# Kernel optimization log

Measured on AMD Instinct MI355X. Metric: run time of the kernel, lower is better.

The kernel has to match this reference:

```python
import jax, jax.numpy as jnp
import numpy as np

N_NODES = 100000
N_EDGES = 1600000
FEAT = 64
HID = 64
N_LAYERS = 3
N_GRAPHS = 500


def setup_inputs() -> dict:
    key = jax.random.key(0)
    ks = jax.random.split(key, 8)
    x = jax.random.normal(ks[0], (N_NODES, FEAT), dtype=jnp.float32)
    edge_index = jax.random.randint(ks[1], (2, N_EDGES), 0, N_NODES, dtype=jnp.int64)
    mask = jax.random.randint(ks[2], (N_NODES,), 0, 2).astype(bool)
    batch = jnp.sort(jax.random.randint(ks[3], (N_NODES,), 0, N_GRAPHS, dtype=jnp.int64))
    Ws = jax.random.normal(ks[4], (N_LAYERS, HID, HID), dtype=jnp.float32) * 0.1
    bs = jnp.zeros((N_LAYERS, HID), dtype=jnp.float32)
    lt1_w = jax.random.normal(ks[5], (HID, 1), dtype=jnp.float32) * 0.1
    lt1_b = jnp.zeros((1,), dtype=jnp.float32)
    return {"x": x, "edge_index": edge_index, "mask": mask, "batch": batch,
            "Ws": Ws, "bs": bs, "lt1_w": lt1_w, "lt1_b": lt1_b}


def reference(x, edge_index, mask, batch, Ws, bs, lt1_w, lt1_b):
    n = x.shape[0]
    self_loop = jnp.arange(n, dtype=edge_index.dtype)
    src = jnp.concatenate([edge_index[0], self_loop])  # [E+N]
    dst = jnp.concatenate([edge_index[1], self_loop])
    # GCN symmetric normalization with self loops
    deg = jax.ops.segment_sum(jnp.ones_like(dst, dtype=x.dtype), dst, num_segments=n)
    dis = jax.lax.rsqrt(deg)  # deg >= 1 thanks to self loops
    norm = (dis[src] * dis[dst])[:, None]  # [E+N, 1]

    h = x
    for i in range(N_LAYERS):
        h = h @ Ws[i]                                   # [N, H] linear (no bias)
        msg = h[src] * norm                              # gather + scale
        h = jax.ops.segment_sum(msg, dst, num_segments=n) + bs[i]  # scatter-add + bias
        h = jax.nn.elu(h)
        # F.dropout with training=False is identity (eval mode)

    # global_mean_pool over masked nodes per graph
    m = mask.astype(h.dtype)
    num = jax.ops.segment_sum(h * m[:, None], batch, num_segments=N_GRAPHS)
    den = jax.ops.segment_sum(m, batch, num_segments=N_GRAPHS)
    pooled = num / jnp.maximum(den, 1.0)[:, None]        # [G, H]
    return pooled @ lt1_w + lt1_b                        # [G, 1]
```

## Files before the change

kernel.cpp:

```cpp
#include <hip/hip_runtime.h>
#include <math.h>

#define N_NODES 100000
#define N_EDGES 1600000
#define HID 64
#define N_LAYERS 3
#define N_GRAPHS 500

#define BUK_SHIFT 9
#define BUK_NODES 512
#define NBUK ((N_NODES + BUK_NODES - 1) / BUK_NODES)
#define BIN_BLOCKS 256
#define CHUNK ((N_EDGES + BIN_BLOCKS - 1) / BIN_BLOCKS)
#define BCAP 16384
#define PCAP 20480

#define TM 64
#define LDX 68

typedef _Float16 half_t;
union H4 { ushort4 u; half_t h[4]; };

__device__ __forceinline__ float elu_f(float x) { return x > 0.f ? x : expm1f(x); }
__device__ __forceinline__ int pad8(int c) { return (c + 7) & ~7; }


__global__ void kA_bin(const int* __restrict__ ei, int* __restrict__ bcur,
                       unsigned int* __restrict__ bin) {
    __shared__ int h[NBUK];
    __shared__ int rsv[NBUK];
    for (int i = threadIdx.x; i < NBUK; i += 256) h[i] = 0;
    __syncthreads();
    int lo = blockIdx.x * CHUNK;
    int hi = min(lo + CHUNK, N_EDGES);
    for (int e = lo + (int)threadIdx.x; e < hi; e += 256)
        atomicAdd(&h[ei[N_EDGES + e] >> BUK_SHIFT], 1);
    __syncthreads();
    for (int i = threadIdx.x; i < NBUK; i += 256) {
        int c = h[i];
        rsv[i] = c ? atomicAdd(&bcur[i], c) : 0;
        h[i] = 0;
    }
    __syncthreads();
    for (int e = lo + (int)threadIdx.x; e < hi; e += 256) {
        int d = ei[N_EDGES + e];
        int s = ei[e];
        int b = d >> BUK_SHIFT;
        int pos = rsv[b] + atomicAdd(&h[b], 1);
        if (pos < BCAP)
            bin[(size_t)b * BCAP + pos] = (unsigned)s | ((unsigned)(d & (BUK_NODES - 1)) << 17);
    }
}

__global__ void kB_build(const unsigned int* __restrict__ bin,
                         const int* __restrict__ bcur,
                         int* __restrict__ poff, int* __restrict__ plen,
                         float* __restrict__ dis, int* __restrict__ psrc,
                         half_t* __restrict__ B16) {
    __shared__ int cnt[BUK_NODES];
    __shared__ int excl[BUK_NODES];
    __shared__ int ps[256];
    int b = blockIdx.x;
    int t = threadIdx.x;
    int ecnt = min(bcur[b], BCAP);
    size_t e0 = (size_t)b * BCAP;
    size_t p0 = (size_t)b * PCAP;
    int n0 = b << BUK_SHIFT;

    if (b == 0 && t < HID) B16[(size_t)N_NODES * HID + t] = (half_t)0.f;

    cnt[t] = 0; cnt[t + 256] = 0;
    __syncthreads();
    for (int e = t; e < ecnt; e += 256)
        atomicAdd(&cnt[bin[e0 + e] >> 17], 1);
    __syncthreads();
    int pc0 = pad8(cnt[2 * t]), pc1 = pad8(cnt[2 * t + 1]);
    int psum = pc0 + pc1;
    ps[t] = psum;
    __syncthreads();
    for (int o = 1; o < 256; o <<= 1) {
        int u = (t >= o) ? ps[t - o] : 0;
        __syncthreads();
        ps[t] += u;
        __syncthreads();
    }
    int pexcl = ps[t] - psum;
    excl[2 * t] = pexcl;
    excl[2 * t + 1] = pexcl + pc0;
    int ptot = ps[255];
    __syncthreads();
    for (int i = t; i < BUK_NODES; i += 256) {
        int n = n0 + i;
        if (n < N_NODES) {
            poff[n] = (int)p0 + excl[i];
            plen[n] = pad8(cnt[i]);
            dis[n] = rsqrtf((float)cnt[i] + 1.0f);
        }
    }
    for (int j = t; j < ptot; j += 256) psrc[p0 + j] = N_NODES;
    __syncthreads();
    cnt[t] = excl[t]; cnt[t + 256] = excl[t + 256];
    __syncthreads();
    for (int e = t; e < ecnt; e += 256) {
        unsigned v = bin[e0 + e];
        int dloc = v >> 17;
        int pos = atomicAdd(&cnt[dloc], 1);
        if (pos < PCAP) psrc[p0 + pos] = (int)(v & 0x1FFFFu);
    }
}


#define FMA4(acc, xs_, wv_) \
    acc.x = fmaf(xs_, wv_.x, acc.x); acc.y = fmaf(xs_, wv_.y, acc.y); \
    acc.z = fmaf(xs_, wv_.z, acc.z); acc.w = fmaf(xs_, wv_.w, acc.w);

__global__ void __launch_bounds__(256, 4)
k_gemm(const float* __restrict__ Xf, const half_t* __restrict__ Xh,
       const float* __restrict__ W, const float* __restrict__ bias, int act,
       const float* __restrict__ dis, half_t* __restrict__ B16, int n) {
    __shared__ float  wsh[HID * LDX];
    __shared__ half_t xs[TM * LDX];
    int t = threadIdx.x;
    int row0 = blockIdx.x * TM;

#pragma unroll
    for (int q = 0; q < 4; q++) {
        int f = q * 1024 + t * 4;
        int r = f >> 6, c = f & 63;
        *(float4*)&wsh[r * LDX + c] = *(const float4*)&W[f];
    }
#pragma unroll
    for (int q = 0; q < 4; q++) {
        int f = q * 1024 + t * 4;
        int r = f >> 6, c = f & 63;
        int gr = row0 + r;
        float4 v = make_float4(0.f, 0.f, 0.f, 0.f);
        if (gr < n) {
            if (act) {
                H4 xu; xu.u = *(const ushort4*)&Xh[(size_t)gr * HID + c];
                float4 bb = *(const float4*)&bias[c];
                v.x = elu_f((float)xu.h[0] + bb.x);
                v.y = elu_f((float)xu.h[1] + bb.y);
                v.z = elu_f((float)xu.h[2] + bb.z);
                v.w = elu_f((float)xu.h[3] + bb.w);
            } else {
                v = *(const float4*)&Xf[(size_t)gr * HID + c];
            }
        }
        H4 pk;
        pk.h[0] = (half_t)v.x; pk.h[1] = (half_t)v.y;
        pk.h[2] = (half_t)v.z; pk.h[3] = (half_t)v.w;
        *(ushort4*)&xs[r * LDX + c] = pk.u;
    }
    __syncthreads();

    int tx = t & 15, ty = t >> 4;
    float4 acc0 = make_float4(0.f, 0.f, 0.f, 0.f);
    float4 acc1 = acc0, acc2 = acc0, acc3 = acc0;

#pragma unroll 1
    for (int k = 0; k < HID; k += 4) {
        float4 w0 = *(const float4*)&wsh[(k + 0) * LDX + 4 * tx];
        float4 w1 = *(const float4*)&wsh[(k + 1) * LDX + 4 * tx];
        float4 w2 = *(const float4*)&wsh[(k + 2) * LDX + 4 * tx];
        float4 w3 = *(const float4*)&wsh[(k + 3) * LDX + 4 * tx];
        {
            H4 xu; xu.u = *(const ushort4*)&xs[(4 * ty + 0) * LDX + k];
            FMA4(acc0, (float)xu.h[0], w0) FMA4(acc0, (float)xu.h[1], w1)
            FMA4(acc0, (float)xu.h[2], w2) FMA4(acc0, (float)xu.h[3], w3)
        }
        {
            H4 xu; xu.u = *(const ushort4*)&xs[(4 * ty + 1) * LDX + k];
            FMA4(acc1, (float)xu.h[0], w0) FMA4(acc1, (float)xu.h[1], w1)
            FMA4(acc1, (float)xu.h[2], w2) FMA4(acc1, (float)xu.h[3], w3)
        }
        {
            H4 xu; xu.u = *(const ushort4*)&xs[(4 * ty + 2) * LDX + k];
            FMA4(acc2, (float)xu.h[0], w0) FMA4(acc2, (float)xu.h[1], w1)
            FMA4(acc2, (float)xu.h[2], w2) FMA4(acc2, (float)xu.h[3], w3)
        }
        {
            H4 xu; xu.u = *(const ushort4*)&xs[(4 * ty + 3) * LDX + k];
            FMA4(acc3, (float)xu.h[0], w0) FMA4(acc3, (float)xu.h[1], w1)
            FMA4(acc3, (float)xu.h[2], w2) FMA4(acc3, (float)xu.h[3], w3)
        }
    }

#pragma unroll
    for (int i = 0; i < 4; i++) {
        float4 a = (i == 0) ? acc0 : (i == 1) ? acc1 : (i == 2) ? acc2 : acc3;
        int gr = row0 + 4 * ty + i;
        if (gr < n) {
            float d = dis[gr];
            H4 pk;
            pk.h[0] = (half_t)(a.x * d); pk.h[1] = (half_t)(a.y * d);
            pk.h[2] = (half_t)(a.z * d); pk.h[3] = (half_t)(a.w * d);
            *(ushort4*)&B16[(size_t)gr * HID + 4 * tx] = pk.u;
        }
    }
}

__global__ void k_agg(const int* __restrict__ poff, const int* __restrict__ plen,
                      const int* __restrict__ psrc,
                      const float* __restrict__ dis, const half_t* __restrict__ B16,
                      half_t* __restrict__ A16, int n) {
    int lane = threadIdx.x & 63;
    int node = __builtin_amdgcn_readfirstlane((blockIdx.x * blockDim.x + threadIdx.x) >> 6);
    if (node >= n) return;
    float acc = (float)B16[(size_t)node * HID + lane];
    int p = poff[node];
    int p1 = p + plen[node];
    for (; p + 16 <= p1; p += 16) {
        int s[16];
#pragma unroll
        for (int i = 0; i < 16; i++) s[i] = psrc[p + i];
        float v[16];
#pragma unroll
        for (int i = 0; i < 16; i++) v[i] = (float)B16[(size_t)s[i] * HID + lane];
        acc += (((v[0] + v[1]) + (v[2] + v[3])) + ((v[4] + v[5]) + (v[6] + v[7])))
             + (((v[8] + v[9]) + (v[10] + v[11])) + ((v[12] + v[13]) + (v[14] + v[15])));
    }
    if (p < p1) {
        int s[8];
#pragma unroll
        for (int i = 0; i < 8; i++) s[i] = psrc[p + i];
        float v[8];
#pragma unroll
        for (int i = 0; i < 8; i++) v[i] = (float)B16[(size_t)s[i] * HID + lane];
        acc += ((v[0] + v[1]) + (v[2] + v[3])) + ((v[4] + v[5]) + (v[6] + v[7]));
    }
    A16[(size_t)node * HID + lane] = (half_t)(acc * dis[node]);
}

__global__ void k_pool_final(const half_t* __restrict__ A16, const float* __restrict__ bias,
                             const int* __restrict__ mask, const int* __restrict__ batch,
                             const float* __restrict__ w, const float* __restrict__ b,
                             float* __restrict__ out) {
    __shared__ float sacc[4][HID];
    __shared__ float scnt[4];
    int g = blockIdx.x;
    int t = threadIdx.x;
    int lane = t & 63;
    int wv = t >> 6;

    int lo = 0, hi = N_NODES;
    while (lo < hi) { int mid = (lo + hi) >> 1; if (batch[mid] < g) lo = mid + 1; else hi = mid; }
    int n0 = lo;
    hi = N_NODES;
    while (lo < hi) { int mid = (lo + hi) >> 1; if (batch[mid] < g + 1) lo = mid + 1; else hi = mid; }
    int n1 = lo;

    float bl = bias[lane];
    float acc0 = 0.f, acc1 = 0.f;
    float cnt0 = 0.f, cnt1 = 0.f;
    int n = n0 + wv;
    for (; n + 4 < n1; n += 8) {
        int m0 = mask[n], m1 = mask[n + 4];
        float v0 = (float)A16[(size_t)n * HID + lane];
        float v1 = (float)A16[(size_t)(n + 4) * HID + lane];
        if (m0) { acc0 += elu_f(v0 + bl); cnt0 += 1.f; }
        if (m1) { acc1 += elu_f(v1 + bl); cnt1 += 1.f; }
    }
    if (n < n1 && mask[n]) { acc0 += elu_f((float)A16[(size_t)n * HID + lane] + bl); cnt0 += 1.f; }
    acc0 += acc1; cnt0 += cnt1;

    sacc[wv][lane] = acc0;
    if (lane == 0) scnt[wv] = cnt0;
    __syncthreads();
    if (wv == 0) {
        float v = sacc[0][lane] + sacc[1][lane] + sacc[2][lane] + sacc[3][lane];
        float c = scnt[0] + scnt[1] + scnt[2] + scnt[3];
        v = v / fmaxf(c, 1.0f) * w[lane];
#pragma unroll
        for (int o = 32; o > 0; o >>= 1) v += __shfl_down(v, o);
        if (lane == 0) out[g] = v + b[0];
    }
}

extern "C" void kernel_launch(void* const* d_in, const int* in_sizes, int n_in,
                              void* d_out, int out_size, void* d_ws, size_t ws_size,
                              hipStream_t stream) {
    const float* x     = (const float*)d_in[0];
    const int*   ei    = (const int*)d_in[1];
    const int*   mask  = (const int*)d_in[2];
    const int*   batch = (const int*)d_in[3];
    const float* Ws    = (const float*)d_in[4];
    const float* bs    = (const float*)d_in[5];
    const float* lw    = (const float*)d_in[6];
    const float* lb    = (const float*)d_in[7];
    float* out = (float*)d_out;

    half_t* A16  = (half_t*)d_ws;
    half_t* B16  = A16 + (size_t)N_NODES * HID;
    float*  dis  = (float*)(B16 + (size_t)(N_NODES + 1) * HID);
    int*    poff = (int*)(dis + N_NODES);
    int*    plen = poff + N_NODES;
    int*    bcur = plen + N_NODES;
    int*    psrc = bcur + NBUK;
    unsigned int* bin = (unsigned int*)(psrc + (size_t)NBUK * PCAP);

    hipMemsetAsync(bcur, 0, NBUK * sizeof(int), stream);

    kA_bin<<<BIN_BLOCKS, 256, 0, stream>>>(ei, bcur, bin);
    kB_build<<<NBUK, 256, 0, stream>>>(bin, bcur, poff, plen, dis, psrc, B16);

    const int gemm_blocks = (N_NODES + TM - 1) / TM;
    const int row_blocks  = (N_NODES + 3) / 4;
    for (int l = 0; l < N_LAYERS; l++) {
        const float* bias_in = (l == 0) ? bs : bs + (l - 1) * HID;
        k_gemm<<<gemm_blocks, 256, 0, stream>>>((l == 0) ? x : nullptr,
                                                (l == 0) ? nullptr : A16,
                                                Ws + (size_t)l * HID * HID,
                                                bias_in, (l == 0) ? 0 : 1,
                                                dis, B16, N_NODES);
        k_agg<<<row_blocks, 256, 0, stream>>>(poff, plen, psrc, dis, B16, A16, N_NODES);
    }

    k_pool_final<<<N_GRAPHS, 256, 0, stream>>>(A16, bs + 2 * HID, mask, batch, lw, lb, out);
}
```

Baseline: 249.4 us.

## Replace scalar FMA GEMM with MFMA 16x16x32 f16 per-wave tiles

Rewrites the per-layer dense transform to use MFMA f16 instructions. Each wave computes a 16-row tile directly from global memory, with no shared-memory staging. A small kernel converts and transposes the weights to f16 once per call so the B fragments load contiguously. The output stores become scattered 2-byte writes per lane instead of packed 8-byte writes, which may cost store efficiency.

```diff
diff --git a/kernel.cpp b/kernel.cpp
--- a/kernel.cpp
+++ b/kernel.cpp
@@ -15,10 +15,9 @@
 #define BCAP 16384
 #define PCAP 20480
 
-#define TM 64
-#define LDX 68
-
 typedef _Float16 half_t;
+typedef __attribute__((ext_vector_type(8))) _Float16 f16x8;
+typedef __attribute__((ext_vector_type(4))) float f32x4;
 union H4 { ushort4 u; half_t h[4]; };
 
 __device__ __forceinline__ float elu_f(float x) { return x > 0.f ? x : expm1f(x); }
@@ -109,94 +108,94 @@
     }
 }
 
-
-#define FMA4(acc, xs_, wv_) \
-    acc.x = fmaf(xs_, wv_.x, acc.x); acc.y = fmaf(xs_, wv_.y, acc.y); \
-    acc.z = fmaf(xs_, wv_.z, acc.z); acc.w = fmaf(xs_, wv_.w, acc.w);
-
-__global__ void __launch_bounds__(256, 4)
-k_gemm(const float* __restrict__ Xf, const half_t* __restrict__ Xh,
-       const float* __restrict__ W, const float* __restrict__ bias, int act,
-       const float* __restrict__ dis, half_t* __restrict__ B16, int n) {
-    __shared__ float  wsh[HID * LDX];
-    __shared__ half_t xs[TM * LDX];
-    int t = threadIdx.x;
-    int row0 = blockIdx.x * TM;
-
-#pragma unroll
-    for (int q = 0; q < 4; q++) {
-        int f = q * 1024 + t * 4;
-        int r = f >> 6, c = f & 63;
-        *(float4*)&wsh[r * LDX + c] = *(const float4*)&W[f];
-    }
-#pragma unroll
-    for (int q = 0; q < 4; q++) {
-        int f = q * 1024 + t * 4;
-        int r = f >> 6, c = f & 63;
-        int gr = row0 + r;
-        float4 v = make_float4(0.f, 0.f, 0.f, 0.f);
-        if (gr < n) {
-            if (act) {
-                H4 xu; xu.u = *(const ushort4*)&Xh[(size_t)gr * HID + c];
-                float4 bb = *(const float4*)&bias[c];
-                v.x = elu_f((float)xu.h[0] + bb.x);
-                v.y = elu_f((float)xu.h[1] + bb.y);
-                v.z = elu_f((float)xu.h[2] + bb.z);
-                v.w = elu_f((float)xu.h[3] + bb.w);
-            } else {
-                v = *(const float4*)&Xf[(size_t)gr * HID + c];
-            }
-        }
-        H4 pk;
-        pk.h[0] = (half_t)v.x; pk.h[1] = (half_t)v.y;
-        pk.h[2] = (half_t)v.z; pk.h[3] = (half_t)v.w;
-        *(ushort4*)&xs[r * LDX + c] = pk.u;
-    }
-    __syncthreads();
-
-    int tx = t & 15, ty = t >> 4;
-    float4 acc0 = make_float4(0.f, 0.f, 0.f, 0.f);
-    float4 acc1 = acc0, acc2 = acc0, acc3 = acc0;
-
-#pragma unroll 1
-    for (int k = 0; k < HID; k += 4) {
-        float4 w0 = *(const float4*)&wsh[(k + 0) * LDX + 4 * tx];
-        float4 w1 = *(const float4*)&wsh[(k + 1) * LDX + 4 * tx];
-        float4 w2 = *(const float4*)&wsh[(k + 2) * LDX + 4 * tx];
-        float4 w3 = *(const float4*)&wsh[(k + 3) * LDX + 4 * tx];
-        {
-            H4 xu; xu.u = *(const ushort4*)&xs[(4 * ty + 0) * LDX + k];
-            FMA4(acc0, (float)xu.h[0], w0) FMA4(acc0, (float)xu.h[1], w1)
-            FMA4(acc0, (float)xu.h[2], w2) FMA4(acc0, (float)xu.h[3], w3)
-        }
-        {
-            H4 xu; xu.u = *(const ushort4*)&xs[(4 * ty + 1) * LDX + k];
-            FMA4(acc1, (float)xu.h[0], w0) FMA4(acc1, (float)xu.h[1], w1)
-            FMA4(acc1, (float)xu.h[2], w2) FMA4(acc1, (float)xu.h[3], w3)
-        }
-        {
-            H4 xu; xu.u = *(const ushort4*)&xs[(4 * ty + 2) * LDX + k];
-            FMA4(acc2, (float)xu.h[0], w0) FMA4(acc2, (float)xu.h[1], w1)
-            FMA4(acc2, (float)xu.h[2], w2) FMA4(acc2, (float)xu.h[3], w3)
-        }
-        {
-            H4 xu; xu.u = *(const ushort4*)&xs[(4 * ty + 3) * LDX + k];
-            FMA4(acc3, (float)xu.h[0], w0) FMA4(acc3, (float)xu.h[1], w1)
-            FMA4(acc3, (float)xu.h[2], w2) FMA4(acc3, (float)xu.h[3], w3)
-        }
-    }
-
-#pragma unroll
-    for (int i = 0; i < 4; i++) {
-        float4 a = (i == 0) ? acc0 : (i == 1) ? acc1 : (i == 2) ? acc2 : acc3;
-        int gr = row0 + 4 * ty + i;
-        if (gr < n) {
-            float d = dis[gr];
-            H4 pk;
-            pk.h[0] = (half_t)(a.x * d); pk.h[1] = (half_t)(a.y * d);
-            pk.h[2] = (half_t)(a.z * d); pk.h[3] = (half_t)(a.w * d);
-            *(ushort4*)&B16[(size_t)gr * HID + 4 * tx] = pk.u;
-        }
+__global__ void k_w16t(const float* __restrict__ Ws, half_t* __restrict__ W16T) {
+    int i = blockIdx.x * 256 + threadIdx.x;
+    if (i >= N_LAYERS * HID * HID) return;
+    int l = i >> 12;
+    int k = (i >> 6) & 63;
+    int c = i & 63;
+    W16T[(size_t)l * 4096 + c * 64 + k] = (half_t)Ws[(size_t)l * 4096 + k * 64 + c];
+}
+
+__device__ __forceinline__ f16x8 make_afrag(const float* Xf, const half_t* Xh,
+                                            const float* bias, int act,
+                                            size_t rowbase, int k) {
+    f16x8 a;
+    if (act) {
+        f16x8 xu = *(const f16x8*)(Xh + rowbase + k);
+        float4 ba = *(const float4*)(bias + k);
+        float4 bb = *(const float4*)(bias + k + 4);
+        a[0] = (half_t)elu_f((float)xu[0] + ba.x);
+        a[1] = (half_t)elu_f((float)xu[1] + ba.y);
+        a[2] = (half_t)elu_f((float)xu[2] + ba.z);
+        a[3] = (half_t)elu_f((float)xu[3] + ba.w);
+        a[4] = (half_t)elu_f((float)xu[4] + bb.x);
+        a[5] = (half_t)elu_f((float)xu[5] + bb.y);
+        a[6] = (half_t)elu_f((float)xu[6] + bb.z);
+        a[7] = (half_t)elu_f((float)xu[7] + bb.w);
+    } else {
+        float4 xa = *(const float4*)(Xf + rowbase + k);
+        float4 xb = *(const float4*)(Xf + rowbase + k + 4);
+        a[0] = (half_t)xa.x; a[1] = (half_t)xa.y;
+        a[2] = (half_t)xa.z; a[3] = (half_t)xa.w;
+        a[4] = (half_t)xb.x; a[5] = (half_t)xb.y;
+        a[6] = (half_t)xb.z; a[7] = (half_t)xb.w;
+    }
+    return a;
+}
+
+__global__ void k_gemm(const float* __restrict__ Xf, const half_t* __restrict__ Xh,
+                       const half_t* __restrict__ wt, const float* __restrict__ bias,
+                       int act, const float* __restrict__ dis,
+                       half_t* __restrict__ B16, int n) {
+    int lane = threadIdx.x & 63;
+    int wid = (blockIdx.x * blockDim.x + threadIdx.x) >> 6;
+    int r0 = wid << 4;
+    if (r0 >= n) return;
+    size_t rowbase = (size_t)(r0 + (lane & 15)) * HID;
+    int goff = (lane >> 4) * 8;
+
+    f16x8 a0 = make_afrag(Xf, Xh, bias, act, rowbase, goff);
+    f16x8 a1 = make_afrag(Xf, Xh, bias, act, rowbase, 32 + goff);
+
+    int wcol = (lane & 15) * HID + goff;
+    f32x4 c0 = {0.f, 0.f, 0.f, 0.f}, c1 = c0, c2 = c0, c3 = c0;
+    {
+        f16x8 b0 = *(const f16x8*)&wt[wcol];
+        f16x8 b1 = *(const f16x8*)&wt[wcol + 32];
+        c0 = __builtin_amdgcn_mfma_f32_16x16x32_f16(a0, b0, c0, 0, 0, 0);
+        c0 = __builtin_amdgcn_mfma_f32_16x16x32_f16(a1, b1, c0, 0, 0, 0);
+    }
+    {
+        f16x8 b0 = *(const f16x8*)&wt[1024 + wcol];
+        f16x8 b1 = *(const f16x8*)&wt[1024 + wcol + 32];
+        c1 = __builtin_amdgcn_mfma_f32_16x16x32_f16(a0, b0, c1, 0, 0, 0);
+        c1 = __builtin_amdgcn_mfma_f32_16x16x32_f16(a1, b1, c1, 0, 0, 0);
+    }
+    {
+        f16x8 b0 = *(const f16x8*)&wt[2048 + wcol];
+        f16x8 b1 = *(const f16x8*)&wt[2048 + wcol + 32];
+        c2 = __builtin_amdgcn_mfma_f32_16x16x32_f16(a0, b0, c2, 0, 0, 0);
+        c2 = __builtin_amdgcn_mfma_f32_16x16x32_f16(a1, b1, c2, 0, 0, 0);
+    }
+    {
+        f16x8 b0 = *(const f16x8*)&wt[3072 + wcol];
+        f16x8 b1 = *(const f16x8*)&wt[3072 + wcol + 32];
+        c3 = __builtin_amdgcn_mfma_f32_16x16x32_f16(a0, b0, c3, 0, 0, 0);
+        c3 = __builtin_amdgcn_mfma_f32_16x16x32_f16(a1, b1, c3, 0, 0, 0);
+    }
+
+    int rg = (lane >> 4) * 4;
+    int col = lane & 15;
+#pragma unroll
+    for (int r = 0; r < 4; r++) {
+        int row = r0 + rg + r;
+        float dv = dis[row];
+        size_t rb = (size_t)row * HID;
+        B16[rb + col]      = (half_t)(c0[r] * dv);
+        B16[rb + 16 + col] = (half_t)(c1[r] * dv);
+        B16[rb + 32 + col] = (half_t)(c2[r] * dv);
+        B16[rb + 48 + col] = (half_t)(c3[r] * dv);
     }
 }
 
@@ -296,21 +295,23 @@
     int*    poff = (int*)(dis + N_NODES);
     int*    plen = poff + N_NODES;
     int*    bcur = plen + N_NODES;
-    int*    psrc = bcur + NBUK;
+    half_t* W16T = (half_t*)(bcur + 200);
+    int*    psrc = (int*)(W16T + (size_t)N_LAYERS * HID * HID);
     unsigned int* bin = (unsigned int*)(psrc + (size_t)NBUK * PCAP);
 
     hipMemsetAsync(bcur, 0, NBUK * sizeof(int), stream);
 
     kA_bin<<<BIN_BLOCKS, 256, 0, stream>>>(ei, bcur, bin);
     kB_build<<<NBUK, 256, 0, stream>>>(bin, bcur, poff, plen, dis, psrc, B16);
-
-    const int gemm_blocks = (N_NODES + TM - 1) / TM;
+    k_w16t<<<(N_LAYERS * HID * HID + 255) / 256, 256, 0, stream>>>(Ws, W16T);
+
+    const int gemm_blocks = (N_NODES / 16 + 3) / 4;
     const int row_blocks  = (N_NODES + 3) / 4;
     for (int l = 0; l < N_LAYERS; l++) {
         const float* bias_in = (l == 0) ? bs : bs + (l - 1) * HID;
         k_gemm<<<gemm_blocks, 256, 0, stream>>>((l == 0) ? x : nullptr,
                                                 (l == 0) ? nullptr : A16,
-                                                Ws + (size_t)l * HID * HID,
+                                                W16T + (size_t)l * HID * HID,
                                                 bias_in, (l == 0) ? 0 : 1,
                                                 dis, B16, N_NODES);
         k_agg<<<row_blocks, 256, 0, stream>>>(poff, plen, psrc, dis, B16, A16, N_NODES);
```

Result: faster. 234.4 us (-6.0%).
